# Kernel tuning notes

Measured on AMD Instinct MI355X. Metric: run time of the kernel, lower is better.

The kernel has to match this reference:

```python
import jax, jax.numpy as jnp
import numpy as np
from jax.ops import segment_sum

N_NODES = 50000
N_EDGES = 800000

def setup_inputs() -> dict:
    key = jax.random.key(0)
    ks = jax.random.split(key, 8)
    def glorot(k, shape):
        fan_in, fan_out = shape
        lim = jnp.sqrt(6.0 / (fan_in + fan_out))
        return jax.random.uniform(k, shape, jnp.float32, -lim, lim)
    return {
        'features': jax.random.normal(ks[0], (N_NODES, 1433), jnp.float32),
        'edge_index': jax.random.randint(ks[1], (2, N_EDGES), 0, N_NODES, jnp.int64),
        'W1': glorot(ks[2], (1433, 256)), 'b1': jnp.zeros((256,), jnp.float32),
        'W2': glorot(ks[3], (256, 32)),  'b2': jnp.zeros((32,), jnp.float32),
        'W3': glorot(ks[4], (32, 7)),    'b3': jnp.zeros((7,), jnp.float32),
    }

def _graph_conv(x, W, b, src, dst, c_src, c_dst, n):
    # DGL GraphConv, norm='both', in_feats > out_feats: weight first, then SpMM.
    h = (x * c_src[:, None]) @ W          # [N, out]
    agg = segment_sum(h[src], dst, num_segments=n)  # sparse neighbor sum
    return agg * c_dst[:, None] + b

def reference(features, edge_index, W1, b1, W2, b2, W3, b3):
    n = features.shape[0]
    src, dst = edge_index[0], edge_index[1]
    ones = jnp.ones((src.shape[0],), jnp.float32)
    deg_out = jnp.maximum(segment_sum(ones, src, num_segments=n), 1.0)
    deg_in = jnp.maximum(segment_sum(ones, dst, num_segments=n), 1.0)
    c_src = jax.lax.rsqrt(deg_out)
    c_dst = jax.lax.rsqrt(deg_in)
    x1 = jax.nn.relu(_graph_conv(features, W1, b1, src, dst, c_src, c_dst, n))
    x2 = jax.nn.relu(_graph_conv(x1, W2, b2, src, dst, c_src, c_dst, n))
    x3 = _graph_conv(x2, W3, b3, src, dst, c_src, c_dst, n)
    return jax.nn.log_softmax(x3, axis=1)
```

## Files before the change

### kernel.cpp

```cpp
#include <hip/hip_runtime.h>
#include <math.h>

typedef unsigned short u16;
typedef unsigned int u32;
typedef __attribute__((ext_vector_type(8))) short bf16x8;
typedef __attribute__((ext_vector_type(4))) float f32x4;
typedef float f32x4u __attribute__((vector_size(16), aligned(4)));

#define NN 50000
#define NE 800000
#define F0 1433
#define KP 1440
#define MP 50048
#define D1 256
#define D2 32
#define NB 196
#define HB 3125
#define SB 3125

__device__ __forceinline__ float bf2f(u16 h) { return __uint_as_float(((u32)h) << 16); }
__device__ __forceinline__ u16 f2bf(float f) {
  u32 u = __float_as_uint(f);
  u32 r = (u + 0x7FFFu + ((u >> 16) & 1u)) >> 16;
  return (u16)r;
}
__device__ __forceinline__ u32 cvtpk(float lo, float hi) {
  u32 r;
  asm("v_cvt_pk_bf16_f32 %0, %1, %2" : "=v"(r) : "v"(lo), "v"(hi));
  return r;
}

__device__ __forceinline__ void gl16(const void* g, void* l) {
  __builtin_amdgcn_global_load_lds((const __attribute__((address_space(1))) u32*)g,
                                   (__attribute__((address_space(3))) u32*)l, 16, 0, 0);
}

__global__ __launch_bounds__(256) void k_hist(const int* __restrict__ ei,
                                              int* __restrict__ cs, int* __restrict__ cd) {
  const int e = blockIdx.x * 256 + threadIdx.x;
  if (e < NE) {
    atomicAdd(&cs[ei[e]], 1);
    atomicAdd(&cd[ei[NE + e]], 1);
  }
}

__global__ __launch_bounds__(256) void k_scan1(const int* __restrict__ cd, int* __restrict__ bsum) {
  __shared__ int sh[256];
  const int t = threadIdx.x;
  const int i = blockIdx.x * 256 + t;
  sh[t] = (i < NN) ? cd[i] : 0;
  __syncthreads();
  for (int o = 128; o > 0; o >>= 1) {
    if (t < o) sh[t] += sh[t + o];
    __syncthreads();
  }
  if (t == 0) bsum[blockIdx.x] = sh[0];
}

__global__ __launch_bounds__(256) void k_scan2(const int* __restrict__ bsum, int* __restrict__ boff) {
  __shared__ int sh[256];
  const int t = threadIdx.x;
  const int v = (t < NB) ? bsum[t] : 0;
  sh[t] = v;
  __syncthreads();
  for (int o = 1; o < 256; o <<= 1) {
    int x = (t >= o) ? sh[t - o] : 0;
    __syncthreads();
    sh[t] += x;
    __syncthreads();
  }
  if (t < NB) boff[t] = sh[t] - v;
}

__global__ __launch_bounds__(256) void k_scan3(const int* __restrict__ cd, const int* __restrict__ cs,
                                               const int* __restrict__ boff,
                                               int* __restrict__ row, int* __restrict__ cur,
                                               float* __restrict__ cdst, float* __restrict__ csrc) {
  __shared__ int sh[256];
  const int t = threadIdx.x;
  const int i = blockIdx.x * 256 + t;
  const int v = (i < NN) ? cd[i] : 0;
  sh[t] = v;
  __syncthreads();
  for (int o = 1; o < 256; o <<= 1) {
    int x = (t >= o) ? sh[t - o] : 0;
    __syncthreads();
    sh[t] += x;
    __syncthreads();
  }
  if (i < NN) {
    const int start = boff[blockIdx.x] + sh[t] - v;
    row[i] = start;
    cur[i] = start;
    if (i == NN - 1) row[NN] = start + v;
    cdst[i] = rsqrtf(fmaxf((float)v, 1.0f));
    csrc[i] = rsqrtf(fmaxf((float)cs[i], 1.0f));
  }
}

__global__ __launch_bounds__(256) void k_scatprep(const int* __restrict__ ei,
                                                  int* __restrict__ cur, int* __restrict__ csr,
                                                  const float* __restrict__ W1, const float* __restrict__ W2,
                                                  u16* __restrict__ W1T, u16* __restrict__ W2T) {
  const int bid = blockIdx.x;
  const int t = threadIdx.x;
  if (bid < SB) {
    const int e = bid * 256 + t;
    if (e < NE) {
      const int d = ei[NE + e];
      const int p = atomicAdd(&cur[d], 1);
      csr[p] = ei[e];
    }
    return;
  }
  const int b = bid - SB;
  if (b < KP) {
    W1T[(size_t)t * KP + b] = (b < F0) ? f2bf(W1[(size_t)b * D1 + t]) : (u16)0;
  } else {
    const int idx = (b - KP) * 256 + t;
    const int k = idx & 255, n = idx >> 8;
    W2T[n * 256 + k] = f2bf(W2[k * 32 + n]);
  }
}

__global__ __launch_bounds__(256) void k_gemm1(const float* __restrict__ F,
                                               const u16* __restrict__ BT,
                                               const float* __restrict__ csrc, u16* __restrict__ H) {
  __shared__ u16 As[128 * 32];
  __shared__ u16 Bs[128 * 32];
  const int tid = threadIdx.x;
  const int wave = tid >> 6, lane = tid & 63;
  const int l16 = lane & 15, quad = lane >> 4;
  const int waveM = wave & 1, waveN = wave >> 1;

  const int wg = blockIdx.x;
  const int xcd = wg & 7, idx = wg >> 3;
  const int swz = (xcd < 6) ? xcd * 98 + idx : 588 + (xcd - 6) * 97 + idx;
  const int tn = swz & 1, tm = swz >> 1;

  f32x4 acc[4][4];
#pragma unroll
  for (int mi = 0; mi < 4; ++mi)
#pragma unroll
    for (int ni = 0; ni < 4; ++ni) acc[mi][ni] = f32x4{0.f, 0.f, 0.f, 0.f};

  const int c0 = wave * 64 + lane;
  const int rA0 = c0 >> 2, qA0 = (c0 & 3) * 8;
  int ga0 = tm * 128 + rA0;        if (ga0 >= NN) ga0 = NN - 1;
  int ga1 = tm * 128 + rA0 + 64;   if (ga1 >= NN) ga1 = NN - 1;
  const float* a0p = F + (size_t)ga0 * F0 + qA0;
  const float* a1p = F + (size_t)ga1 * F0 + qA0;
  const bool fix0 = (ga0 == NN - 1) && (qA0 == 24);
  const bool fix1 = (ga1 == NN - 1) && (qA0 == 24);

  const u16* Bb = BT + (size_t)tn * 128 * KP;
  u16* Bs0 = Bs + (wave * 64) * 8;
  u16* Bs1 = Bs + (wave * 64 + 256) * 8;
  const size_t offB0 = (size_t)rA0 * KP + qA0;
  const size_t offB1 = (size_t)(rA0 + 64) * KP + qA0;
  uint4* As0w = (uint4*)As + c0;
  uint4* As1w = (uint4*)As + (c0 + 256);

  f32x4u va0 = *(const f32x4u*)(a0p);
  f32x4u vb0 = *(const f32x4u*)(a0p + 4);
  f32x4u va1 = *(const f32x4u*)(a1p);
  f32x4u vb1 = *(const f32x4u*)(a1p + 4);

  for (int kt = 0; kt < KP / 32; ++kt) {
    const int k0 = kt * 32;
    __syncthreads();
    uint4 w0, w1;
    w0.x = cvtpk(va0[0], va0[1]); w0.y = cvtpk(va0[2], va0[3]);
    w0.z = cvtpk(vb0[0], vb0[1]); w0.w = cvtpk(vb0[2], vb0[3]);
    w1.x = cvtpk(va1[0], va1[1]); w1.y = cvtpk(va1[2], va1[3]);
    w1.z = cvtpk(vb1[0], vb1[1]); w1.w = cvtpk(vb1[2], vb1[3]);
    *As0w = w0;
    *As1w = w1;
    gl16(Bb + offB0 + k0, Bs0);
    gl16(Bb + offB1 + k0, Bs1);
    __syncthreads();
    if (kt < 44) {
      const int kn = k0 + 32;
      va0 = *(const f32x4u*)(a0p + kn); vb0 = *(const f32x4u*)(a0p + kn + 4);
      va1 = *(const f32x4u*)(a1p + kn); vb1 = *(const f32x4u*)(a1p + kn + 4);
      if (kt == 43) {
        if (fix0) {
          float lastv = F[(size_t)(NN - 1) * F0 + 1432];
          va0[0] = lastv; va0[1] = 0.f; va0[2] = 0.f; va0[3] = 0.f;
          vb0[0] = 0.f;   vb0[1] = 0.f; vb0[2] = 0.f; vb0[3] = 0.f;
        }
        if (fix1) {
          float lastv = F[(size_t)(NN - 1) * F0 + 1432];
          va1[0] = lastv; va1[1] = 0.f; va1[2] = 0.f; va1[3] = 0.f;
          vb1[0] = 0.f;   vb1[1] = 0.f; vb1[2] = 0.f; vb1[3] = 0.f;
        }
      }
    }
    bf16x8 af[4], bfr[4];
#pragma unroll
    for (int mi = 0; mi < 4; ++mi)
      af[mi] = *(const bf16x8*)(As + ((waveM * 64 + mi * 16 + l16) * 32 + quad * 8));
#pragma unroll
    for (int ni = 0; ni < 4; ++ni)
      bfr[ni] = *(const bf16x8*)(Bs + ((waveN * 64 + ni * 16 + l16) * 32 + quad * 8));
#pragma unroll
    for (int mi = 0; mi < 4; ++mi)
#pragma unroll
      for (int ni = 0; ni < 4; ++ni)
        acc[mi][ni] = __builtin_amdgcn_mfma_f32_16x16x32_bf16(af[mi], bfr[ni], acc[mi][ni], 0, 0, 0);
  }

  const int rbase = tm * 128 + waveM * 64 + quad * 4;
  const int cbase = tn * 128 + waveN * 64 + l16;
#pragma unroll
  for (int mi = 0; mi < 4; ++mi) {
#pragma unroll
    for (int e = 0; e < 4; ++e) {
      const int i = rbase + mi * 16 + e;
      if (i < NN) {
        const float cs = csrc[i];
#pragma unroll
        for (int ni = 0; ni < 4; ++ni)
          H[(size_t)i * D1 + cbase + ni * 16] = f2bf(acc[mi][ni][e] * cs);
      }
    }
  }
}

__global__ __launch_bounds__(256) void k_spmm1f(const int* __restrict__ row, const int* __restrict__ csr,
                                                const u16* __restrict__ h1, const float* __restrict__ cdst,
                                                const float* __restrict__ csrc, const float* __restrict__ b1,
                                                u16* __restrict__ x) {
  const int d = blockIdx.x * 4 + (threadIdx.x >> 6);
  const int lane = threadIdx.x & 63;
  const int rs = row[d], re = row[d + 1];
  float a0 = 0.f, a1 = 0.f, a2 = 0.f, a3 = 0.f;
  int e = rs;
  for (; e + 3 < re; e += 4) {
    const int s0 = csr[e], s1 = csr[e + 1], s2 = csr[e + 2], s3 = csr[e + 3];
    const ushort4 v0 = *(const ushort4*)(h1 + (size_t)s0 * D1 + lane * 4);
    const ushort4 v1 = *(const ushort4*)(h1 + (size_t)s1 * D1 + lane * 4);
    const ushort4 v2 = *(const ushort4*)(h1 + (size_t)s2 * D1 + lane * 4);
    const ushort4 v3 = *(const ushort4*)(h1 + (size_t)s3 * D1 + lane * 4);
    a0 += (bf2f(v0.x) + bf2f(v1.x)) + (bf2f(v2.x) + bf2f(v3.x));
    a1 += (bf2f(v0.y) + bf2f(v1.y)) + (bf2f(v2.y) + bf2f(v3.y));
    a2 += (bf2f(v0.z) + bf2f(v1.z)) + (bf2f(v2.z) + bf2f(v3.z));
    a3 += (bf2f(v0.w) + bf2f(v1.w)) + (bf2f(v2.w) + bf2f(v3.w));
  }
  for (; e < re; ++e) {
    const int s0 = csr[e];
    const ushort4 v0 = *(const ushort4*)(h1 + (size_t)s0 * D1 + lane * 4);
    a0 += bf2f(v0.x); a1 += bf2f(v0.y); a2 += bf2f(v0.z); a3 += bf2f(v0.w);
  }
  const float cd = cdst[d], cs = csrc[d];
  const float4 bb = *(const float4*)(b1 + lane * 4);
  const float r0 = fmaxf(a0 * cd + bb.x, 0.f) * cs;
  const float r1 = fmaxf(a1 * cd + bb.y, 0.f) * cs;
  const float r2 = fmaxf(a2 * cd + bb.z, 0.f) * cs;
  const float r3 = fmaxf(a3 * cd + bb.w, 0.f) * cs;
  ushort4 o;
  o.x = f2bf(r0); o.y = f2bf(r1); o.z = f2bf(r2); o.w = f2bf(r3);
  *(ushort4*)(x + (size_t)d * D1 + lane * 4) = o;
}

__global__ __launch_bounds__(256) void k_gemm2(const u16* __restrict__ A, const u16* __restrict__ BT,
                                               u16* __restrict__ H) {
  __shared__ u16 As[128 * 32];
  __shared__ u16 Bs[32 * 32];
  const int tid = threadIdx.x;
  const int wave = tid >> 6, lane = tid & 63;
  const int l16 = lane & 15, quad = lane >> 4;
  const int tm = blockIdx.x;

  f32x4 acc[2][2];
#pragma unroll
  for (int mi = 0; mi < 2; ++mi)
#pragma unroll
    for (int ni = 0; ni < 2; ++ni) acc[mi][ni] = f32x4{0.f, 0.f, 0.f, 0.f};

  const int r0 = tid >> 2, q0 = (tid & 3) * 8;
  int rowA0 = tm * 128 + r0;      if (rowA0 >= NN) rowA0 = NN - 1;
  int rowA1 = tm * 128 + r0 + 64; if (rowA1 >= NN) rowA1 = NN - 1;
  for (int kt = 0; kt < 8; ++kt) {
    const int k0 = kt * 32;
    __syncthreads();
    uint4 v0 = *(const uint4*)(A + (size_t)rowA0 * D1 + k0 + q0);
    uint4 v1 = *(const uint4*)(A + (size_t)rowA1 * D1 + k0 + q0);
    *(uint4*)(As + r0 * 32 + q0) = v0;
    *(uint4*)(As + (r0 + 64) * 32 + q0) = v1;
    if (tid < 128) {
      uint4 vb = *(const uint4*)(BT + (size_t)r0 * D1 + k0 + q0);
      *(uint4*)(Bs + r0 * 32 + q0) = vb;
    }
    __syncthreads();
    bf16x8 af[2], bfr[2];
#pragma unroll
    for (int mi = 0; mi < 2; ++mi)
      af[mi] = *(const bf16x8*)(As + ((wave * 32 + mi * 16 + l16) * 32 + quad * 8));
#pragma unroll
    for (int ni = 0; ni < 2; ++ni)
      bfr[ni] = *(const bf16x8*)(Bs + ((ni * 16 + l16) * 32 + quad * 8));
#pragma unroll
    for (int mi = 0; mi < 2; ++mi)
#pragma unroll
      for (int ni = 0; ni < 2; ++ni)
        acc[mi][ni] = __builtin_amdgcn_mfma_f32_16x16x32_bf16(af[mi], bfr[ni], acc[mi][ni], 0, 0, 0);
  }

  const int rbase = tm * 128 + wave * 32 + quad * 4;
#pragma unroll
  for (int mi = 0; mi < 2; ++mi)
#pragma unroll
    for (int e = 0; e < 4; ++e) {
      const int i = rbase + mi * 16 + e;
      if (i < NN) {
#pragma unroll
        for (int ni = 0; ni < 2; ++ni)
          H[(size_t)i * D2 + ni * 16 + l16] = f2bf(acc[mi][ni][e]);
      }
    }
}

__global__ __launch_bounds__(256) void k_spmm2f(const int* __restrict__ row, const int* __restrict__ csr,
                                                const u16* __restrict__ h2, const float* __restrict__ cdst,
                                                const float* __restrict__ csrc, const float* __restrict__ b2,
                                                u16* __restrict__ x) {
  const int t = threadIdx.x;
  const int d = blockIdx.x * 8 + (t >> 5);
  const int f = t & 31;
  const int rs = row[d], re = row[d + 1];
  float acc = 0.f;
  int e = rs;
  for (; e + 3 < re; e += 4) {
    const int s0 = csr[e], s1 = csr[e + 1], s2 = csr[e + 2], s3 = csr[e + 3];
    acc += (bf2f(h2[(size_t)s0 * D2 + f]) + bf2f(h2[(size_t)s1 * D2 + f])) +
           (bf2f(h2[(size_t)s2 * D2 + f]) + bf2f(h2[(size_t)s3 * D2 + f]));
  }
  for (; e < re; ++e) acc += bf2f(h2[(size_t)csr[e] * D2 + f]);
  const float v = acc * cdst[d] + b2[f];
  x[(size_t)d * D2 + f] = f2bf(fmaxf(v, 0.f) * csrc[d]);
}

__global__ __launch_bounds__(256) void k_l3(const u16* __restrict__ x, const float* __restrict__ W3,
                                            float* __restrict__ h3) {
  __shared__ float w3s[224];
  const int t = threadIdx.x;
  if (t < 224) w3s[t] = W3[t];
  __syncthreads();
  const int i = blockIdx.x * 256 + t;
  if (i >= NN) return;
  const uint4* p = (const uint4*)(x + (size_t)i * D2);
  union { uint4 v[4]; u16 s[32]; } u;
  u.v[0] = p[0]; u.v[1] = p[1]; u.v[2] = p[2]; u.v[3] = p[3];
  float acc[7];
#pragma unroll
  for (int c = 0; c < 7; ++c) acc[c] = 0.f;
#pragma unroll
  for (int k = 0; k < 32; ++k) {
    const float xv = bf2f(u.s[k]);
#pragma unroll
    for (int c = 0; c < 7; ++c) acc[c] += xv * w3s[k * 7 + c];
  }
  float* o = h3 + (size_t)i * 8;
#pragma unroll
  for (int c = 0; c < 7; ++c) o[c] = acc[c];
}

__global__ __launch_bounds__(256) void k_spmm3f(const int* __restrict__ row, const int* __restrict__ csr,
                                                const float* __restrict__ h3, const float* __restrict__ cdst,
                                                const float* __restrict__ b3, float* __restrict__ out) {
  const int t = threadIdx.x;
  const int d = blockIdx.x * 32 + (t >> 3);
  const int c = t & 7;
  if (d >= NN) return;
  const int rs = row[d], re = row[d + 1];
  float acc = 0.f;
  if (c < 7) {
    int e = rs;
    for (; e + 1 < re; e += 2)
      acc += h3[(size_t)csr[e] * 8 + c] + h3[(size_t)csr[e + 1] * 8 + c];
    if (e < re) acc += h3[(size_t)csr[e] * 8 + c];
  }
  const float v = (c < 7) ? (acc * cdst[d] + b3[c]) : -INFINITY;
  float m = v;
  m = fmaxf(m, __shfl_xor(m, 1));
  m = fmaxf(m, __shfl_xor(m, 2));
  m = fmaxf(m, __shfl_xor(m, 4));
  float s = (c < 7) ? expf(v - m) : 0.f;
  s += __shfl_xor(s, 1);
  s += __shfl_xor(s, 2);
  s += __shfl_xor(s, 4);
  const float l = logf(s);
  if (c < 7) out[(size_t)d * 7 + c] = v - m - l;
}

static const size_t O_CSRC = 0;
static const size_t O_CDST = 200192;
static const size_t O_ROW  = 400384;
static const size_t O_CUR  = 601088;
static const size_t O_CNTS = 801792;
static const size_t O_CNTD = 1002496;
static const size_t O_BSUM = 1203200;
static const size_t O_BOFF = 1204224;
static const size_t O_CSR  = 1205248;
static const size_t O_W1T  = 4405248;
static const size_t O_W2T  = 5142528;
static const size_t O_H1   = 5158912;
static const size_t O_X1S  = 30758912;
static const size_t O_H2   = O_X1S + 25600000;
static const size_t O_X2S  = O_X1S + 28800000;
static const size_t O_H3   = O_X1S + 32000000;

extern "C" void kernel_launch(void* const* d_in, const int* in_sizes, int n_in,
                              void* d_out, int out_size, void* d_ws, size_t ws_size,
                              hipStream_t stream) {
  const float* feat = (const float*)d_in[0];
  const int* ei     = (const int*)d_in[1];
  const float* W1   = (const float*)d_in[2];
  const float* b1   = (const float*)d_in[3];
  const float* W2   = (const float*)d_in[4];
  const float* b2   = (const float*)d_in[5];
  const float* W3   = (const float*)d_in[6];
  const float* b3   = (const float*)d_in[7];
  float* out = (float*)d_out;

  char* ws = (char*)d_ws;
  float* c_src = (float*)(ws + O_CSRC);
  float* c_dst = (float*)(ws + O_CDST);
  int* row  = (int*)(ws + O_ROW);
  int* cur  = (int*)(ws + O_CUR);
  int* cnts = (int*)(ws + O_CNTS);
  int* cntd = (int*)(ws + O_CNTD);
  int* bsum = (int*)(ws + O_BSUM);
  int* boff = (int*)(ws + O_BOFF);
  int* csr  = (int*)(ws + O_CSR);
  u16* W1T  = (u16*)(ws + O_W1T);
  u16* W2T  = (u16*)(ws + O_W2T);
  u16* h1   = (u16*)(ws + O_H1);
  u16* x1s  = (u16*)(ws + O_X1S);
  u16* h2   = (u16*)(ws + O_H2);
  u16* x2s  = (u16*)(ws + O_X2S);
  float* h3 = (float*)(ws + O_H3);

  hipMemsetAsync(cnts, 0, (size_t)NN * 4, stream);
  hipMemsetAsync(cntd, 0, (size_t)NN * 4, stream);
  k_hist<<<HB, 256, 0, stream>>>(ei, cnts, cntd);
  k_scan1<<<NB, 256, 0, stream>>>(cntd, bsum);
  k_scan2<<<1, 256, 0, stream>>>(bsum, boff);
  k_scan3<<<NB, 256, 0, stream>>>(cntd, cnts, boff, row, cur, c_dst, c_src);
  k_scatprep<<<SB + KP + 32, 256, 0, stream>>>(ei, cur, csr, W1, W2, W1T, W2T);

  k_gemm1<<<782, 256, 0, stream>>>(feat, W1T, c_src, h1);
  k_spmm1f<<<NN / 4, 256, 0, stream>>>(row, csr, h1, c_dst, c_src, b1, x1s);

  k_gemm2<<<MP / 128, 256, 0, stream>>>(x1s, W2T, h2);
  k_spmm2f<<<NN / 8, 256, 0, stream>>>(row, csr, h2, c_dst, c_src, b2, x2s);

  k_l3<<<(NN + 255) / 256, 256, 0, stream>>>(x2s, W3, h3);
  k_spmm3f<<<(NN + 31) / 32, 256, 0, stream>>>(row, csr, h3, c_dst, b3, out);
}
```

Measured before the change: 710.3 us.

## Double K-tile depth in first GEMM and XOR-swizzle shared memory layout

The first dense GEMM now processes 64-wide K tiles instead of 32, padding K to 1472, which halves the number of barrier-separated iterations and doubles the MFMA work per sync. Shared-memory tiles for A and B use an XOR swizzle on 16-byte chunks to avoid LDS bank conflicts on the fragment reads. The tail handling for the last row's out-of-bounds columns and the workspace offsets are adjusted to match. The cost is larger LDS usage and more live registers for the prefetched A rows, which may reduce occupancy.

```diff
diff --git a/kernel.cpp b/kernel.cpp
--- a/kernel.cpp
+++ b/kernel.cpp
@@ -10,7 +10,8 @@
 #define NN 50000
 #define NE 800000
 #define F0 1433
-#define KP 1440
+#define KP2 1472
+#define KT1 23
 #define MP 50048
 #define D1 256
 #define D2 32
@@ -114,10 +115,10 @@
     return;
   }
   const int b = bid - SB;
-  if (b < KP) {
-    W1T[(size_t)t * KP + b] = (b < F0) ? f2bf(W1[(size_t)b * D1 + t]) : (u16)0;
+  if (b < KP2) {
+    W1T[(size_t)t * KP2 + b] = (b < F0) ? f2bf(W1[(size_t)b * D1 + t]) : (u16)0;
   } else {
-    const int idx = (b - KP) * 256 + t;
+    const int idx = (b - KP2) * 256 + t;
     const int k = idx & 255, n = idx >> 8;
     W2T[n * 256 + k] = f2bf(W2[k * 32 + n]);
   }
@@ -126,8 +127,8 @@
 __global__ __launch_bounds__(256) void k_gemm1(const float* __restrict__ F,
                                                const u16* __restrict__ BT,
                                                const float* __restrict__ csrc, u16* __restrict__ H) {
-  __shared__ u16 As[128 * 32];
-  __shared__ u16 Bs[128 * 32];
+  __shared__ u16 As[128 * 64];
+  __shared__ u16 Bs[128 * 64];
   const int tid = threadIdx.x;
   const int wave = tid >> 6, lane = tid & 63;
   const int l16 = lane & 15, quad = lane >> 4;
@@ -144,70 +145,87 @@
 #pragma unroll
     for (int ni = 0; ni < 4; ++ni) acc[mi][ni] = f32x4{0.f, 0.f, 0.f, 0.f};
 
-  const int c0 = wave * 64 + lane;
-  const int rA0 = c0 >> 2, qA0 = (c0 & 3) * 8;
-  int ga0 = tm * 128 + rA0;        if (ga0 >= NN) ga0 = NN - 1;
-  int ga1 = tm * 128 + rA0 + 64;   if (ga1 >= NN) ga1 = NN - 1;
-  const float* a0p = F + (size_t)ga0 * F0 + qA0;
-  const float* a1p = F + (size_t)ga1 * F0 + qA0;
-  const bool fix0 = (ga0 == NN - 1) && (qA0 == 24);
-  const bool fix1 = (ga1 == NN - 1) && (qA0 == 24);
-
-  const u16* Bb = BT + (size_t)tn * 128 * KP;
-  u16* Bs0 = Bs + (wave * 64) * 8;
-  u16* Bs1 = Bs + (wave * 64 + 256) * 8;
-  const size_t offB0 = (size_t)rA0 * KP + qA0;
-  const size_t offB1 = (size_t)(rA0 + 64) * KP + qA0;
-  uint4* As0w = (uint4*)As + c0;
-  uint4* As1w = (uint4*)As + (c0 + 256);
-
-  f32x4u va0 = *(const f32x4u*)(a0p);
-  f32x4u vb0 = *(const f32x4u*)(a0p + 4);
-  f32x4u va1 = *(const f32x4u*)(a1p);
-  f32x4u vb1 = *(const f32x4u*)(a1p + 4);
-
-  for (int kt = 0; kt < KP / 32; ++kt) {
-    const int k0 = kt * 32;
-    __syncthreads();
-    uint4 w0, w1;
-    w0.x = cvtpk(va0[0], va0[1]); w0.y = cvtpk(va0[2], va0[3]);
-    w0.z = cvtpk(vb0[0], vb0[1]); w0.w = cvtpk(vb0[2], vb0[3]);
-    w1.x = cvtpk(va1[0], va1[1]); w1.y = cvtpk(va1[2], va1[3]);
-    w1.z = cvtpk(vb1[0], vb1[1]); w1.w = cvtpk(vb1[2], vb1[3]);
-    *As0w = w0;
-    *As1w = w1;
-    gl16(Bb + offB0 + k0, Bs0);
-    gl16(Bb + offB1 + k0, Bs1);
-    __syncthreads();
-    if (kt < 44) {
-      const int kn = k0 + 32;
-      va0 = *(const f32x4u*)(a0p + kn); vb0 = *(const f32x4u*)(a0p + kn + 4);
-      va1 = *(const f32x4u*)(a1p + kn); vb1 = *(const f32x4u*)(a1p + kn + 4);
-      if (kt == 43) {
-        if (fix0) {
-          float lastv = F[(size_t)(NN - 1) * F0 + 1432];
-          va0[0] = lastv; va0[1] = 0.f; va0[2] = 0.f; va0[3] = 0.f;
-          vb0[0] = 0.f;   vb0[1] = 0.f; vb0[2] = 0.f; vb0[3] = 0.f;
-        }
-        if (fix1) {
-          float lastv = F[(size_t)(NN - 1) * F0 + 1432];
-          va1[0] = lastv; va1[1] = 0.f; va1[2] = 0.f; va1[3] = 0.f;
-          vb1[0] = 0.f;   vb1[1] = 0.f; vb1[2] = 0.f; vb1[3] = 0.f;
+  const int ko = (tid & 7) * 8;
+  const int rx = (tid >> 3) & 7;
+  const int wlow = (tid & 7) ^ rx;
+
+  int lastm = 0;
+  const float* ap[4];
+#pragma unroll
+  for (int j = 0; j < 4; ++j) {
+    const int r = (tid >> 3) + 32 * j;
+    int g = tm * 128 + r;
+    if (g == NN - 1) lastm |= (1 << j);
+    if (g >= NN) g = 0;
+    ap[j] = F + (size_t)g * F0 + ko;
+  }
+
+  const u16* Bb = BT + (size_t)(tn * 128) * KP2;
+  size_t bofs[4];
+#pragma unroll
+  for (int j = 0; j < 4; ++j)
+    bofs[j] = (size_t)((tid >> 3) + 32 * j) * KP2 + wlow * 8;
+
+  uint4* Asw = (uint4*)As;
+
+  f32x4u va[4], vb[4];
+#pragma unroll
+  for (int j = 0; j < 4; ++j) {
+    va[j] = *(const f32x4u*)(ap[j]);
+    vb[j] = *(const f32x4u*)(ap[j] + 4);
+  }
+
+  for (int kt = 0; kt < KT1; ++kt) {
+    const int k0 = kt * 64;
+    __syncthreads();
+#pragma unroll
+    for (int j = 0; j < 4; ++j) {
+      uint4 w;
+      w.x = cvtpk(va[j][0], va[j][1]); w.y = cvtpk(va[j][2], va[j][3]);
+      w.z = cvtpk(vb[j][0], vb[j][1]); w.w = cvtpk(vb[j][2], vb[j][3]);
+      Asw[((tid + 256 * j) & ~7) | wlow] = w;
+    }
+#pragma unroll
+    for (int j = 0; j < 4; ++j)
+      gl16(Bb + bofs[j] + k0, (uint4*)Bs + (wave * 64 + 256 * j));
+    __syncthreads();
+    if (kt < KT1 - 1) {
+      const int kn = k0 + 64;
+      const bool tail = (kn == (KT1 - 1) * 64);
+#pragma unroll
+      for (int j = 0; j < 4; ++j) {
+        if (tail && ((lastm >> j) & 1) && ko >= 24) {
+          f32x4u z = {0.f, 0.f, 0.f, 0.f};
+          f32x4u t0 = z;
+          if (ko == 24) t0[0] = F[(size_t)NN * F0 - 1];
+          va[j] = t0;
+          vb[j] = z;
+        } else {
+          va[j] = *(const f32x4u*)(ap[j] + kn);
+          vb[j] = *(const f32x4u*)(ap[j] + kn + 4);
         }
       }
     }
-    bf16x8 af[4], bfr[4];
-#pragma unroll
-    for (int mi = 0; mi < 4; ++mi)
-      af[mi] = *(const bf16x8*)(As + ((waveM * 64 + mi * 16 + l16) * 32 + quad * 8));
-#pragma unroll
-    for (int ni = 0; ni < 4; ++ni)
-      bfr[ni] = *(const bf16x8*)(Bs + ((waveN * 64 + ni * 16 + l16) * 32 + quad * 8));
-#pragma unroll
-    for (int mi = 0; mi < 4; ++mi)
-#pragma unroll
-      for (int ni = 0; ni < 4; ++ni)
-        acc[mi][ni] = __builtin_amdgcn_mfma_f32_16x16x32_bf16(af[mi], bfr[ni], acc[mi][ni], 0, 0, 0);
+#pragma unroll
+    for (int ks = 0; ks < 2; ++ks) {
+      const int cq = ks * 4 + quad;
+      bf16x8 af[4], bfr[4];
+#pragma unroll
+      for (int mi = 0; mi < 4; ++mi) {
+        const int r = waveM * 64 + mi * 16 + l16;
+        af[mi] = *(const bf16x8*)(As + r * 64 + ((cq ^ (r & 7)) << 3));
+      }
+#pragma unroll
+      for (int ni = 0; ni < 4; ++ni) {
+        const int r = waveN * 64 + ni * 16 + l16;
+        bfr[ni] = *(const bf16x8*)(Bs + r * 64 + ((cq ^ (r & 7)) << 3));
+      }
+#pragma unroll
+      for (int mi = 0; mi < 4; ++mi)
+#pragma unroll
+        for (int ni = 0; ni < 4; ++ni)
+          acc[mi][ni] = __builtin_amdgcn_mfma_f32_16x16x32_bf16(af[mi], bfr[ni], acc[mi][ni], 0, 0, 0);
+    }
   }
 
   const int rbase = tm * 128 + waveM * 64 + quad * 4;
@@ -404,12 +422,12 @@
 static const size_t O_BOFF = 1204224;
 static const size_t O_CSR  = 1205248;
 static const size_t O_W1T  = 4405248;
-static const size_t O_W2T  = 5142528;
-static const size_t O_H1   = 5158912;
-static const size_t O_X1S  = 30758912;
-static const size_t O_H2   = O_X1S + 25600000;
-static const size_t O_X2S  = O_X1S + 28800000;
-static const size_t O_H3   = O_X1S + 32000000;
+static const size_t O_W2T  = 5158912;
+static const size_t O_H1   = 5175296;
+static const size_t O_X1S  = 30775296;
+static const size_t O_H2   = 56375296;
+static const size_t O_X2S  = 59575296;
+static const size_t O_H3   = 62775296;
 
 extern "C" void kernel_launch(void* const* d_in, const int* in_sizes, int n_in,
                               void* d_out, int out_size, void* d_ws, size_t ws_size,
@@ -448,7 +466,7 @@
   k_scan1<<<NB, 256, 0, stream>>>(cntd, bsum);
   k_scan2<<<1, 256, 0, stream>>>(bsum, boff);
   k_scan3<<<NB, 256, 0, stream>>>(cntd, cnts, boff, row, cur, c_dst, c_src);
-  k_scatprep<<<SB + KP + 32, 256, 0, stream>>>(ei, cur, csr, W1, W2, W1T, W2T);
+  k_scatprep<<<SB + KP2 + 32, 256, 0, stream>>>(ei, cur, csr, W1, W2, W1T, W2T);
 
   k_gemm1<<<782, 256, 0, stream>>>(feat, W1T, c_src, h1);
   k_spmm1f<<<NN / 4, 256, 0, stream>>>(row, csr, h1, c_dst, c_src, b1, x1s);
```

Result: faster. 693.1 us (-2.4%).
